# Kernel tuning notes

Measured on AMD Instinct MI355X. Metric: run time of the kernel, lower is better.

The kernel has to match this reference:

```python
import jax, jax.numpy as jnp
import numpy as np

N, D = 1024, 64  # n_nodes, inputSize == hiddenSize == cellSize


def setup_inputs() -> dict:
    key = jax.random.key(0)
    ks = jax.random.split(key, 9)
    inputs = jax.random.normal(ks[0], (N, D), dtype=jnp.float32)
    # sparse-ish binary adjacency, no self loops
    adj = (jax.random.uniform(ks[1], (N, N)) < 0.03).astype(jnp.float32)
    adj = adj.at[jnp.arange(N), jnp.arange(N)].set(0.0)
    numNei = jnp.maximum(adj.sum(axis=1), 1.0)  # avoid div-by-zero
    # initStates() in torch uses randn for h0/c0
    h0 = jax.random.normal(ks[2], (N, D), dtype=jnp.float32)
    c0 = jax.random.normal(ks[3], (N, D), dtype=jnp.float32)
    # torch nn.Linear default init: U(-1/sqrt(fan_in), 1/sqrt(fan_in))
    s_g = 1.0 / np.sqrt(2 * D)
    s_h = 1.0 / np.sqrt(D)
    Wg = jax.random.uniform(ks[4], (D, 2 * D), minval=-s_g, maxval=s_g, dtype=jnp.float32)
    bg = jax.random.uniform(ks[5], (D,), minval=-s_g, maxval=s_g, dtype=jnp.float32)
    Ws = jax.random.uniform(ks[6], (D, D), minval=-s_h, maxval=s_h, dtype=jnp.float32)
    bs = jax.random.uniform(ks[7], (D,), minval=-s_h, maxval=s_h, dtype=jnp.float32)
    Wn = jax.random.uniform(ks[8], (D, D), minval=-s_h, maxval=s_h, dtype=jnp.float32)
    sequence = jnp.arange(N, dtype=jnp.int32)
    return {"inputs": inputs, "neighbour": adj, "numNei": numNei,
            "h0": h0, "c0": c0, "Wg": Wg, "bg": bg, "Ws": Ws, "bs": bs,
            "Wn": Wn, "sequence": sequence}


def reference(inputs, neighbour, numNei, h0, c0, Wg, bg, Ws, bs, Wn, sequence):
    def step(carry, idx):
        H, C = carry                       # [N, D] each
        inp = inputs[idx]                  # [D]
        h_i = H[idx]                       # [D]
        c_i = C[idx]                       # [D] (torch passes cellState[index])
        nei = neighbour[idx]               # [N] adjacency row
        num = numNei[idx]
        # neighbour-averaged hidden state
        neiH = (nei @ H) / num             # [D]
        pre = jnp.concatenate([inp, h_i]) @ Wg.T + bg + neiH @ Wn.T  # [D]
        inputState = jax.nn.sigmoid(pre)
        outputState = inputState           # identical expression in torch
        helpCell = jnp.tanh(pre)
        fs = inp @ Ws.T + bs               # selfGate(inp), [D]
        # forgetSelfMat broadcast of fs over all nodes
        neiForget = jax.nn.sigmoid(fs[None, :] + H @ Wn.T)   # [N, D]
        forgetState = jax.nn.sigmoid(fs + h_i @ Wn.T)        # [D]
        c_new = (nei @ (neiForget * c_i[None, :])) / num \
                + forgetState * c_i + inputState * helpCell  # [D]
        h_new = jnp.tanh(outputState * c_new)
        return (H.at[idx].set(h_new), C.at[idx].set(c_new)), None

    (Hf, _Cf), _ = jax.lax.scan(step, (h0, c0), sequence)
    # torch: residualHidden aliases hiddenState and is mutated in-place,
    # so `hiddenState + residualHidden` == 2 * final hidden state.
    return Hf + Hf
```

## Files before the change

### kernel.cpp

```cpp
#include <hip/hip_runtime.h>

#define NN 1024
#define DD 64
#define CAP 96
#define RCAP 128
#define SENT 32768
#define NL2E -1.44269504088896f

typedef __attribute__((ext_vector_type(8))) short bf16x8;
typedef __attribute__((ext_vector_type(4))) float f32x4;

__device__ float    WgTd[128*64];
__device__ float    WsTd[64*64];
__device__ float    WnTd[64*64];
__device__ uint4    WnFragD[8*64];
__device__ float    FSd[NN*DD];
__device__ float    Gd[NN*DD];
__device__ float    preBaseD[NN*DD];
__device__ float    fpreD[NN*DD];
__device__ float4   nodeDatD[NN*DD];
__device__ int      lowNeiD[NN*CAP + 64];
__device__ int      revNeiD[NN*RCAP];
__device__ int      revCntD[NN];
__device__ int2     hdrD[NN];
__device__ int      posArr[NN];
__device__ float    invNumD[NN];

__device__ __forceinline__ float sigm(float x)  { return 1.0f / (1.0f + __expf(-x)); }
__device__ __forceinline__ float tanhf_(float x){ return 2.0f / (1.0f + __expf(-2.0f*x)) - 1.0f; }
__device__ __forceinline__ unsigned short bf16r(float x) {
  unsigned u = __float_as_uint(x);
  u = u + 0x7fffu + ((u >> 16) & 1u);
  return (unsigned short)(u >> 16);
}

__global__ __launch_bounds__(256) void k_prep(const int* __restrict__ seq,
                                              const float* __restrict__ numNei,
                                              const float* __restrict__ Wg,
                                              const float* __restrict__ Ws,
                                              const float* __restrict__ Wn) {
  int gid = blockIdx.x * 256 + threadIdx.x;
  if (gid < NN) { posArr[seq[gid]] = gid; invNumD[gid] = 1.0f / numNei[gid]; revCntD[gid] = 0; }
  if (gid < 512) {
    int st = gid >> 6, lane = gid & 63;
    int s = st >> 2, t = st & 3;
    int row = 16*t + (lane & 15);
    int k0 = 32*s + 8*(lane >> 4);
    const float* wr = &Wn[row*64 + k0];
    uint4 f;
    f.x = (unsigned)bf16r(wr[0]) | ((unsigned)bf16r(wr[1]) << 16);
    f.y = (unsigned)bf16r(wr[2]) | ((unsigned)bf16r(wr[3]) << 16);
    f.z = (unsigned)bf16r(wr[4]) | ((unsigned)bf16r(wr[5]) << 16);
    f.w = (unsigned)bf16r(wr[6]) | ((unsigned)bf16r(wr[7]) << 16);
    WnFragD[st*64 + lane] = f;
  }
  for (int e = gid; e < NN*CAP; e += 64*256) lowNeiD[e] = SENT;
  if (gid < 128*64) {
    int d = gid >> 7, k = gid & 127;
    WgTd[k*64 + d] = Wg[gid];
  } else if (gid < 128*64 + 64*64) {
    int idx = gid - 128*64; int d = idx >> 6, k = idx & 63;
    WsTd[k*64 + d] = Ws[idx];
  } else {
    int idx = gid - (128*64 + 64*64); int d = idx >> 6, k = idx & 63;
    WnTd[k*64 + d] = Wn[idx];
  }
}

__global__ __launch_bounds__(256) void k_node(const float* __restrict__ inputs,
                                              const float* __restrict__ h0,
                                              const float* __restrict__ bg,
                                              const float* __restrict__ bs) {
  __shared__ float WsT_l[64*64];
  __shared__ float WnT_l[64*64];
  __shared__ float x_l[4][64];
  __shared__ float hh_l[4][64];
  int tid = threadIdx.x;
  for (int idx = tid; idx < 64*64; idx += 256) { WsT_l[idx] = WsTd[idx]; WnT_l[idx] = WnTd[idx]; }
  int w = tid >> 6, d = tid & 63;
  int i = blockIdx.x * 4 + w;
  x_l[w][d]  = inputs[i*DD + d];
  hh_l[w][d] = h0[i*DD + d];
  __syncthreads();
  float afs = bs[d], apre = bg[d], ag0 = 0.0f;
  #pragma unroll 16
  for (int k = 0; k < 64; ++k) {
    float xk = x_l[w][k], hk = hh_l[w][k];
    afs  += xk * WsT_l[k*64 + d];
    ag0  += hk * WnT_l[k*64 + d];
    apre += xk * WgTd[k*64 + d] + hk * WgTd[(64 + k)*64 + d];
  }
  FSd[i*DD + d]      = afs;
  Gd[i*DD + d]       = ag0;
  preBaseD[i*DD + d] = apre;
  fpreD[i*DD + d]    = sigm(afs + ag0);
}

__global__ __launch_bounds__(256) void k_edges(const float* __restrict__ adj,
                                               const float* __restrict__ c0) {
  int tid = threadIdx.x;
  int w = tid >> 6, d = tid & 63;
  int i = blockIdx.x * 4 + w;
  int pi = posArr[i];
  float fs = FSd[i*DD + d];
  float accP = 0.0f, accS = 0.0f;
  int cnt = 0;
  for (int base = 0; base < NN; base += 64) {
    float a = adj[i*NN + base + d];
    unsigned long long mask = __ballot(a != 0.0f);
    while (mask) {
      int b = __ffsll(mask) - 1;
      mask &= (mask - 1);
      int j = base + b;
      if (posArr[j] < pi) {
        if (d == 0 && cnt < 64) {
          lowNeiD[i*CAP + cnt] = j << 5;
          int slot = atomicAdd(&revCntD[j], 1);
          if (slot < RCAP) revNeiD[j*RCAP + slot] = i;
        }
        cnt++;
      } else {
        float g = Gd[j*DD + d];
        accP += g;
        accS += sigm(fs + g);
      }
    }
  }
  float inv = invNumD[i];
  if (d == 0) {
    int ccap = (cnt < 64) ? cnt : 64;
    hdrD[i] = make_int2(ccap, __float_as_int(inv));
  }
  float c0v = c0[i*DD + d];
  float civ = c0v * inv;
  nodeDatD[i*DD + d] = make_float4(NL2E * fs,
                                   preBaseD[i*DD + d] + accP * inv,
                                   civ,
                                   c0v * fpreD[i*DD + d] + civ * accS);
}

__global__ __launch_bounds__(1024, 4) void k_seq(float* __restrict__ out) {
  __shared__ unsigned long long Gl64[(NN*DD + 64)/4];
  __shared__ unsigned low8p[NN][4];
  __shared__ int      queue_[NN];
  __shared__ int      indeg[NN];
  __shared__ float    invL[NN];
  __shared__ unsigned short hstage[16][64];
  __shared__ int head, tail;
  unsigned short* Gl = (unsigned short*)Gl64;
  int tid  = threadIdx.x;
  int lane = tid & 63, w = tid >> 6;
  if (tid == 0) { head = 0; tail = 0; }
  queue_[tid] = -1;
  int2 hdr = hdrD[tid];
  int  rc  = revCntD[tid];
  int  cnt0 = hdr.x;
  indeg[tid] = cnt0 | (cnt0 << 8) | (rc << 15);
  invL[tid]  = __int_as_float(hdr.y);
  {
    uint4 a = *(const uint4*)&lowNeiD[tid*CAP];
    uint4 b = *(const uint4*)&lowNeiD[tid*CAP + 4];
    low8p[tid][0] = (a.x & 0xffffu) | (a.y << 16);
    low8p[tid][1] = (a.z & 0xffffu) | (a.w << 16);
    low8p[tid][2] = (b.x & 0xffffu) | (b.y << 16);
    low8p[tid][3] = (b.z & 0xffffu) | (b.w << 16);
  }
  if (tid < 16) Gl64[NN*DD/4 + tid] = 0ull;
  uint4 fb[2][4];
  #pragma unroll
  for (int s = 0; s < 2; ++s) {
    #pragma unroll
    for (int t = 0; t < 4; ++t)
      fb[s][t] = WnFragD[(s*4 + t)*64 + lane];
  }
  __syncthreads();
  if (cnt0 == 0) {
    int p = __hip_atomic_fetch_add(&tail, 1, __ATOMIC_RELAXED, __HIP_MEMORY_SCOPE_WORKGROUP);
    __hip_atomic_store(&queue_[p], tid | (rc << 17), __ATOMIC_RELEASE, __HIP_MEMORY_SCOPE_WORKGROUP);
  }
  __syncthreads();

  int t0 = 0;
  if (lane == 0) t0 = __hip_atomic_fetch_add(&head, 1, __ATOMIC_RELAXED, __HIP_MEMORY_SCOPE_WORKGROUP);
  int t = __builtin_amdgcn_readfirstlane(t0);
  int e = -1;
  if (t < NN) {
    e = __hip_atomic_load(&queue_[t], __ATOMIC_ACQUIRE, __HIP_MEMORY_SCOPE_WORKGROUP);
    while (e < 0)
      e = __hip_atomic_load(&queue_[t], __ATOMIC_ACQUIRE, __HIP_MEMORY_SCOPE_WORKGROUP);
  } else {
    return;
  }
  e = __builtin_amdgcn_readfirstlane(e);

  int    i, cnt, rcnt, jb2v, r0, r1;
  float4 nd;
  float  inv;
  uint4  lvv;
  #define ISSUE(E) do {                                               \
    i    = (E) & 1023;                                                \
    cnt  = ((E) >> 10) & 127;                                         \
    rcnt = ((E) >> 17) & 255;                                         \
    nd   = nodeDatD[i*DD + lane];                                     \
    jb2v = lowNeiD[i*CAP + 8 + lane];                                 \
    r0   = (lane < rcnt)      ? revNeiD[i*RCAP + lane]      : -1;     \
    r1   = (lane + 64 < rcnt) ? revNeiD[i*RCAP + 64 + lane] : -1;     \
    inv  = invL[i];                                                   \
    lvv  = *(uint4*)&low8p[i][0];                                     \
  } while (0)
  ISSUE(e);

  for (;;) {
    float fs2n = nd.x;
    float accG = 0.0f, accS = 0.0f;
    float g0[8], g1[8], g2[8], g3[8];
    #define LD(c) __uint_as_float(((unsigned)Gl[((c) << 1) + lane]) << 16)
    if (cnt > 0) {
      unsigned v0=lvv.x&0xffffu, v1=lvv.x>>16, v2=lvv.y&0xffffu, v3=lvv.y>>16;
      unsigned v4=lvv.z&0xffffu, v5=lvv.z>>16, v6=lvv.w&0xffffu, v7=lvv.w>>16;
      g0[0]=LD(v0); g0[1]=LD(v1); g0[2]=LD(v2); g0[3]=LD(v3);
      g0[4]=LD(v4); g0[5]=LD(v5); g0[6]=LD(v6); g0[7]=LD(v7);
    }
    if (cnt > 8) {
      #pragma unroll
      for (int q = 0; q < 8; ++q) g1[q] = LD(__builtin_amdgcn_readlane(jb2v, q));
    }
    if (cnt > 16) {
      #pragma unroll
      for (int q = 0; q < 8; ++q) g2[q] = LD(__builtin_amdgcn_readlane(jb2v, 8 + q));
    }
    if (cnt > 24) {
      #pragma unroll
      for (int q = 0; q < 8; ++q) g3[q] = LD(__builtin_amdgcn_readlane(jb2v, 16 + q));
    }
    auto domath = [&](float G) {
      float x_ = __builtin_fmaf(G, NL2E, fs2n);
      float e_ = __builtin_amdgcn_exp2f(x_);
      accS += __builtin_amdgcn_rcpf(1.0f + e_);
      accG += G;
    };
    if (cnt > 0) {
      #pragma unroll
      for (int q = 0; q < 8; ++q) domath(g0[q]);
    }
    if (cnt > 8) {
      #pragma unroll
      for (int q = 0; q < 8; ++q) domath(g1[q]);
    }
    if (cnt > 16) {
      #pragma unroll
      for (int q = 0; q < 8; ++q) domath(g2[q]);
    }
    if (cnt > 24) {
      #pragma unroll
      for (int q = 0; q < 8; ++q) domath(g3[q]);
    }
    if (cnt > 32) {
      for (int base = 32; base < cnt; base += 8) {
        float gg[8];
        #pragma unroll
        for (int q = 0; q < 8; ++q) gg[q] = LD(__builtin_amdgcn_readlane(jb2v, base - 8 + q));
        #pragma unroll
        for (int q = 0; q < 8; ++q) domath(gg[q]);
      }
    }
    {
      int nb8 = (cnt + 7) & ~7;
      float sig0 = __builtin_amdgcn_rcpf(1.0f + __builtin_amdgcn_exp2f(fs2n));
      accS -= (float)(nb8 - cnt) * sig0;
    }
    float pre = nd.y + inv * accG;
    float is  = sigm(pre);
    float hcl = tanhf_(pre);
    float c   = nd.z * accS + nd.w + is * hcl;
    float h   = tanhf_(is * c);
    int ic = i, r0c = r0, r1c = r1;
    if (lane == 0) t0 = __hip_atomic_fetch_add(&head, 1, __ATOMIC_RELAXED, __HIP_MEMORY_SCOPE_WORKGROUP);
    t = __builtin_amdgcn_readfirstlane(t0);
    bool done = (t >= NN);
    int e2 = -1;
    if (!done) e2 = __hip_atomic_load(&queue_[t], __ATOMIC_ACQUIRE, __HIP_MEMORY_SCOPE_WORKGROUP);
    e2 = __builtin_amdgcn_readfirstlane(e2);
    bool pre_ok = (e2 >= 0);
    if (pre_ok) ISSUE(e2);
    hstage[w][lane] = bf16r(h);
    const uint4* hv = (const uint4*)&hstage[w][0];
    uint4 fa0 = hv[lane >> 4];
    uint4 fa1 = hv[4 + (lane >> 4)];
    f32x4 z = {0.f, 0.f, 0.f, 0.f};
    f32x4 a0 = __builtin_amdgcn_mfma_f32_16x16x32_bf16(__builtin_bit_cast(bf16x8, fa0), __builtin_bit_cast(bf16x8, fb[0][0]), z, 0, 0, 0);
    f32x4 a1 = __builtin_amdgcn_mfma_f32_16x16x32_bf16(__builtin_bit_cast(bf16x8, fa0), __builtin_bit_cast(bf16x8, fb[0][1]), z, 0, 0, 0);
    f32x4 a2 = __builtin_amdgcn_mfma_f32_16x16x32_bf16(__builtin_bit_cast(bf16x8, fa0), __builtin_bit_cast(bf16x8, fb[0][2]), z, 0, 0, 0);
    f32x4 a3 = __builtin_amdgcn_mfma_f32_16x16x32_bf16(__builtin_bit_cast(bf16x8, fa0), __builtin_bit_cast(bf16x8, fb[0][3]), z, 0, 0, 0);
    a0 = __builtin_amdgcn_mfma_f32_16x16x32_bf16(__builtin_bit_cast(bf16x8, fa1), __builtin_bit_cast(bf16x8, fb[1][0]), a0, 0, 0, 0);
    a1 = __builtin_amdgcn_mfma_f32_16x16x32_bf16(__builtin_bit_cast(bf16x8, fa1), __builtin_bit_cast(bf16x8, fb[1][1]), a1, 0, 0, 0);
    a2 = __builtin_amdgcn_mfma_f32_16x16x32_bf16(__builtin_bit_cast(bf16x8, fa1), __builtin_bit_cast(bf16x8, fb[1][2]), a2, 0, 0, 0);
    a3 = __builtin_amdgcn_mfma_f32_16x16x32_bf16(__builtin_bit_cast(bf16x8, fa1), __builtin_bit_cast(bf16x8, fb[1][3]), a3, 0, 0, 0);
    float r01 = (lane & 16) ? a1[0] : a0[0];
    float r23 = (lane & 16) ? a3[0] : a2[0];
    float rg  = (lane & 32) ? r23 : r01;
    Gl[(ic << 6) + lane] = bf16r(rg);
    if (r0c >= 0) {
      int old = __hip_atomic_fetch_add(&indeg[r0c], -1, __ATOMIC_ACQ_REL, __HIP_MEMORY_SCOPE_WORKGROUP);
      if ((old & 0xff) == 1) {
        int p = __hip_atomic_fetch_add(&tail, 1, __ATOMIC_RELAXED, __HIP_MEMORY_SCOPE_WORKGROUP);
        int en = r0c | (((old >> 8) & 127) << 10) | (((old >> 15) & 255) << 17);
        __hip_atomic_store(&queue_[p], en, __ATOMIC_RELEASE, __HIP_MEMORY_SCOPE_WORKGROUP);
      }
    }
    if (r1c >= 0) {
      int old = __hip_atomic_fetch_add(&indeg[r1c], -1, __ATOMIC_ACQ_REL, __HIP_MEMORY_SCOPE_WORKGROUP);
      if ((old & 0xff) == 1) {
        int p = __hip_atomic_fetch_add(&tail, 1, __ATOMIC_RELAXED, __HIP_MEMORY_SCOPE_WORKGROUP);
        int en = r1c | (((old >> 8) & 127) << 10) | (((old >> 15) & 255) << 17);
        __hip_atomic_store(&queue_[p], en, __ATOMIC_RELEASE, __HIP_MEMORY_SCOPE_WORKGROUP);
      }
    }
    out[ic*DD + lane] = 2.0f * h;
    if (done) break;
    if (!pre_ok) {
      int e3 = __hip_atomic_load(&queue_[t], __ATOMIC_ACQUIRE, __HIP_MEMORY_SCOPE_WORKGROUP);
      while (e3 < 0)
        e3 = __hip_atomic_load(&queue_[t], __ATOMIC_ACQUIRE, __HIP_MEMORY_SCOPE_WORKGROUP);
      e3 = __builtin_amdgcn_readfirstlane(e3);
      ISSUE(e3);
    }
  }
  #undef LD
  #undef ISSUE
}

extern "C" void kernel_launch(void* const* d_in, const int* in_sizes, int n_in,
                              void* d_out, int out_size, void* d_ws, size_t ws_size,
                              hipStream_t stream) {
  const float* inputs = (const float*)d_in[0];
  const float* adj    = (const float*)d_in[1];
  const float* numNei = (const float*)d_in[2];
  const float* h0     = (const float*)d_in[3];
  const float* c0     = (const float*)d_in[4];
  const float* Wg     = (const float*)d_in[5];
  const float* bg     = (const float*)d_in[6];
  const float* Ws     = (const float*)d_in[7];
  const float* bs     = (const float*)d_in[8];
  const float* Wn     = (const float*)d_in[9];
  const int*   seq    = (const int*)d_in[10];
  float* out = (float*)d_out;

  k_prep <<<64, 256, 0, stream>>>(seq, numNei, Wg, Ws, Wn);
  k_node <<<256, 256, 0, stream>>>(inputs, h0, bg, bs);
  k_edges<<<256, 256, 0, stream>>>(adj, c0);
  k_seq  <<<1, 1024, 0, stream>>>(out);
}
```

Measured before the change: 208.4 us.

## Fuse prep into node kernel and prefetch newly-ready nodes' data in sequential loop

Merges the prep kernel into the per-node projection kernel. The weights are now read directly from global as float4 rows instead of through transposed global copies staged in shared memory, which removes one launch and the transpose traffic. In the single-block sequential kernel, the first two nodes pushed to the ready queue each step get their nodeDat and neighbour-list rows loaded early into registers kept alive with an empty asm statement, to warm the cache ahead of their ISSUE. The prefetch adds extra loads and registers to the critical serial loop, and the row-wise weight reads are strided across lanes.

Measured after the change: 216.6 us. 3.9% more time.

```diff
diff --git a/kernel.cpp b/kernel.cpp
--- a/kernel.cpp
+++ b/kernel.cpp
@@ -10,9 +10,6 @@
 typedef __attribute__((ext_vector_type(8))) short bf16x8;
 typedef __attribute__((ext_vector_type(4))) float f32x4;
 
-__device__ float    WgTd[128*64];
-__device__ float    WsTd[64*64];
-__device__ float    WnTd[64*64];
 __device__ uint4    WnFragD[8*64];
 __device__ float    FSd[NN*DD];
 __device__ float    Gd[NN*DD];
@@ -34,12 +31,19 @@
   return (unsigned short)(u >> 16);
 }
 
-__global__ __launch_bounds__(256) void k_prep(const int* __restrict__ seq,
+__global__ __launch_bounds__(256) void k_node(const int* __restrict__ seq,
                                               const float* __restrict__ numNei,
+                                              const float* __restrict__ inputs,
+                                              const float* __restrict__ h0,
                                               const float* __restrict__ Wg,
+                                              const float* __restrict__ bg,
                                               const float* __restrict__ Ws,
+                                              const float* __restrict__ bs,
                                               const float* __restrict__ Wn) {
-  int gid = blockIdx.x * 256 + threadIdx.x;
+  __shared__ float x_l[4][64];
+  __shared__ float hh_l[4][64];
+  int tid = threadIdx.x;
+  int gid = blockIdx.x * 256 + tid;
   if (gid < NN) { posArr[seq[gid]] = gid; invNumD[gid] = 1.0f / numNei[gid]; revCntD[gid] = 0; }
   if (gid < 512) {
     int st = gid >> 6, lane = gid & 63;
@@ -54,41 +58,32 @@
     f.w = (unsigned)bf16r(wr[6]) | ((unsigned)bf16r(wr[7]) << 16);
     WnFragD[st*64 + lane] = f;
   }
-  for (int e = gid; e < NN*CAP; e += 64*256) lowNeiD[e] = SENT;
-  if (gid < 128*64) {
-    int d = gid >> 7, k = gid & 127;
-    WgTd[k*64 + d] = Wg[gid];
-  } else if (gid < 128*64 + 64*64) {
-    int idx = gid - 128*64; int d = idx >> 6, k = idx & 63;
-    WsTd[k*64 + d] = Ws[idx];
-  } else {
-    int idx = gid - (128*64 + 64*64); int d = idx >> 6, k = idx & 63;
-    WnTd[k*64 + d] = Wn[idx];
-  }
-}
-
-__global__ __launch_bounds__(256) void k_node(const float* __restrict__ inputs,
-                                              const float* __restrict__ h0,
-                                              const float* __restrict__ bg,
-                                              const float* __restrict__ bs) {
-  __shared__ float WsT_l[64*64];
-  __shared__ float WnT_l[64*64];
-  __shared__ float x_l[4][64];
-  __shared__ float hh_l[4][64];
-  int tid = threadIdx.x;
-  for (int idx = tid; idx < 64*64; idx += 256) { WsT_l[idx] = WsTd[idx]; WnT_l[idx] = WnTd[idx]; }
+  for (int e2 = gid; e2 < NN*CAP; e2 += 256*256) lowNeiD[e2] = SENT;
   int w = tid >> 6, d = tid & 63;
   int i = blockIdx.x * 4 + w;
   x_l[w][d]  = inputs[i*DD + d];
   hh_l[w][d] = h0[i*DD + d];
   __syncthreads();
   float afs = bs[d], apre = bg[d], ag0 = 0.0f;
-  #pragma unroll 16
-  for (int k = 0; k < 64; ++k) {
-    float xk = x_l[w][k], hk = hh_l[w][k];
-    afs  += xk * WsT_l[k*64 + d];
-    ag0  += hk * WnT_l[k*64 + d];
-    apre += xk * WgTd[k*64 + d] + hk * WgTd[(64 + k)*64 + d];
+  const float4* wsr = (const float4*)&Ws[d*64];
+  const float4* wnr = (const float4*)&Wn[d*64];
+  const float4* wga = (const float4*)&Wg[d*128];
+  const float4* wgb = (const float4*)&Wg[d*128 + 64];
+  #pragma unroll 4
+  for (int k4 = 0; k4 < 16; ++k4) {
+    float4 ws4 = wsr[k4], wn4 = wnr[k4], wa4 = wga[k4], wb4 = wgb[k4];
+    const float* wsp = (const float*)&ws4;
+    const float* wnp = (const float*)&wn4;
+    const float* wap = (const float*)&wa4;
+    const float* wbp = (const float*)&wb4;
+    #pragma unroll
+    for (int j = 0; j < 4; ++j) {
+      int k = 4*k4 + j;
+      float xk = x_l[w][k], hk = hh_l[w][k];
+      afs  += xk * wsp[j];
+      ag0  += hk * wnp[j];
+      apre += xk * wap[j] + hk * wbp[j];
+    }
   }
   FSd[i*DD + d]      = afs;
   Gd[i*DD + d]       = ag0;
@@ -210,7 +205,13 @@
   } while (0)
   ISSUE(e);
 
+  float4 tA0 = {0,0,0,0}, tA1 = {0,0,0,0};
+  int    tB0 = 0, tB1 = 0;
+
   for (;;) {
+    asm volatile("" :: "v"(tA0.x), "v"(tA0.y), "v"(tA0.z), "v"(tA0.w),
+                       "v"(tA1.x), "v"(tA1.y), "v"(tA1.z), "v"(tA1.w),
+                       "v"(tB0), "v"(tB1));
     float fs2n = nd.x;
     float accG = 0.0f, accS = 0.0f;
     float g0[8], g1[8], g2[8], g3[8];
@@ -300,12 +301,14 @@
     float r23 = (lane & 16) ? a3[0] : a2[0];
     float rg  = (lane & 32) ? r23 : r01;
     Gl[(ic << 6) + lane] = bf16r(rg);
+    int push0 = -1, push1 = -1;
     if (r0c >= 0) {
       int old = __hip_atomic_fetch_add(&indeg[r0c], -1, __ATOMIC_ACQ_REL, __HIP_MEMORY_SCOPE_WORKGROUP);
       if ((old & 0xff) == 1) {
         int p = __hip_atomic_fetch_add(&tail, 1, __ATOMIC_RELAXED, __HIP_MEMORY_SCOPE_WORKGROUP);
         int en = r0c | (((old >> 8) & 127) << 10) | (((old >> 15) & 255) << 17);
         __hip_atomic_store(&queue_[p], en, __ATOMIC_RELEASE, __HIP_MEMORY_SCOPE_WORKGROUP);
+        push0 = r0c;
       }
     }
     if (r1c >= 0) {
@@ -314,6 +317,32 @@
         int p = __hip_atomic_fetch_add(&tail, 1, __ATOMIC_RELAXED, __HIP_MEMORY_SCOPE_WORKGROUP);
         int en = r1c | (((old >> 8) & 127) << 10) | (((old >> 15) & 255) << 17);
         __hip_atomic_store(&queue_[p], en, __ATOMIC_RELEASE, __HIP_MEMORY_SCOPE_WORKGROUP);
+        push1 = r1c;
+      }
+    }
+    {
+      unsigned long long pm0 = __ballot(push0 >= 0);
+      unsigned long long pm1 = __ballot(push1 >= 0);
+      int rdA = -1, rdB = -1;
+      if (pm0) {
+        int b = __ffsll(pm0) - 1;
+        rdA = __builtin_amdgcn_readlane(push0, b);
+        pm0 &= (pm0 - 1);
+      }
+      if (pm0) {
+        int b = __ffsll(pm0) - 1;
+        rdB = __builtin_amdgcn_readlane(push0, b);
+      } else if (pm1) {
+        int b = __ffsll(pm1) - 1;
+        rdB = __builtin_amdgcn_readlane(push1, b);
+      }
+      if (rdA >= 0) {
+        tA0 = nodeDatD[rdA*DD + lane];
+        tB0 = lowNeiD[rdA*CAP + 8 + lane];
+      }
+      if (rdB >= 0) {
+        tA1 = nodeDatD[rdB*DD + lane];
+        tB1 = lowNeiD[rdB*CAP + 8 + lane];
       }
     }
     out[ic*DD + lane] = 2.0f * h;
@@ -346,8 +375,7 @@
   const int*   seq    = (const int*)d_in[10];
   float* out = (float*)d_out;
 
-  k_prep <<<64, 256, 0, stream>>>(seq, numNei, Wg, Ws, Wn);
-  k_node <<<256, 256, 0, stream>>>(inputs, h0, bg, bs);
+  k_node <<<256, 256, 0, stream>>>(seq, numNei, inputs, h0, Wg, bg, Ws, bs, Wn);
   k_edges<<<256, 256, 0, stream>>>(adj, c0);
   k_seq  <<<1, 1024, 0, stream>>>(out);
 }
```
